# Optimization experiments

Hardware: AMD Instinct MI355X
Metric: run time of the kernel (lower is better)

## Reference

```python
import jax, jax.numpy as jnp
import numpy as np

STRIDES = (4, 8, 16, 32, 64)
RATIOS = (0.5, 1.0, 2.0)
SCALE = 8.0
A = 3
PRE_NMS = 2000
MAX_PER_IMG = 1000
NMS_THR = 0.7
MAX_RATIO = float(abs(np.log(16.0 / 1000.0)))  # wh_ratio_clip = 16/1000
LEVEL_OFFSET = 4096.0  # > max image coordinate, separates levels for batched NMS
FEAT_HW = ((208, 336), (104, 168), (52, 84), (26, 42), (13, 21))
N = 8


def grid_anchors(stride, H, W):
    # mmdet-style base anchors: scale 8, ratios (0.5,1,2), centered at 0
    r = jnp.asarray(RATIOS, jnp.float32)
    h_r = jnp.sqrt(r)
    w_r = 1.0 / h_r
    ws = stride * w_r * SCALE
    hs = stride * h_r * SCALE
    base = jnp.stack([-ws / 2, -hs / 2, ws / 2, hs / 2], axis=-1)  # [A,4]
    sx = jnp.arange(W, dtype=jnp.float32) * stride
    sy = jnp.arange(H, dtype=jnp.float32) * stride
    yy, xx = jnp.meshgrid(sy, sx, indexing='ij')
    shifts = jnp.stack([xx, yy, xx, yy], axis=-1).reshape(-1, 4)  # [H*W,4], row-major
    return (shifts[:, None, :] + base[None, :, :]).reshape(-1, 4)  # [H*W*A,4]


def decode(anchors, deltas, h, w):
    # DeltaXYWH decode with means 0, stds 1, clip to image
    px = (anchors[..., 0] + anchors[..., 2]) * 0.5
    py = (anchors[..., 1] + anchors[..., 3]) * 0.5
    pw = anchors[..., 2] - anchors[..., 0]
    ph = anchors[..., 3] - anchors[..., 1]
    dx, dy = deltas[..., 0], deltas[..., 1]
    dw = jnp.clip(deltas[..., 2], -MAX_RATIO, MAX_RATIO)
    dh = jnp.clip(deltas[..., 3], -MAX_RATIO, MAX_RATIO)
    gx = px + pw * dx
    gy = py + ph * dy
    gw = pw * jnp.exp(dw)
    gh = ph * jnp.exp(dh)
    x1 = jnp.clip(gx - gw * 0.5, 0.0, w)
    y1 = jnp.clip(gy - gh * 0.5, 0.0, h)
    x2 = jnp.clip(gx + gw * 0.5, 0.0, w)
    y2 = jnp.clip(gy + gh * 0.5, 0.0, h)
    return jnp.stack([x1, y1, x2, y2], axis=-1)


def iou_matrix(b):
    area = (b[:, 2] - b[:, 0]) * (b[:, 3] - b[:, 1])
    lt = jnp.maximum(b[:, None, :2], b[None, :, :2])
    rb = jnp.minimum(b[:, None, 2:], b[None, :, 2:])
    wh = jnp.clip(rb - lt, 0.0, None)
    inter = wh[..., 0] * wh[..., 1]
    union = area[:, None] + area[None, :] - inter
    return inter / jnp.maximum(union, 1e-6)


def _forward(cls_list, reg_list, image_h, image_w):
    scores_all, deltas_all, anchors_all, levels_all = [], [], [], []
    for lvl, (cls, reg) in enumerate(zip(cls_list, reg_list)):
        n, _, H, W = cls.shape
        anchors = grid_anchors(STRIDES[lvl], H, W)  # [H*W*A,4]
        s = jax.nn.sigmoid(jnp.transpose(cls, (0, 2, 3, 1)).reshape(n, -1))
        d = jnp.transpose(reg, (0, 2, 3, 1)).reshape(n, -1, 4)
        k = min(PRE_NMS, s.shape[1])  # topk pre-selection per level
        sv, si = jax.lax.top_k(s, k)
        dv = jnp.take_along_axis(d, si[..., None], axis=1)
        av = anchors[si]
        scores_all.append(sv)
        deltas_all.append(dv)
        anchors_all.append(av)
        levels_all.append(jnp.full((k,), lvl, jnp.int32))
    scores = jnp.concatenate(scores_all, axis=1)    # [N,M]
    deltas = jnp.concatenate(deltas_all, axis=1)    # [N,M,4]
    anchors = jnp.concatenate(anchors_all, axis=1)  # [N,M,4]
    levels = jnp.concatenate(levels_all)            # [M] (same per image)
    boxes = decode(anchors, deltas, float(image_h), float(image_w))
    # filter_boxes with min_area = prod((0,0)) = 0: keep boxes with area >= 0
    area = (boxes[..., 2] - boxes[..., 0]) * (boxes[..., 3] - boxes[..., 1])
    scores = jnp.where(area >= 0.0, scores, -1.0)
    M = boxes.shape[1]
    idxs = jnp.arange(M)

    def nms_one(bs):
        b_i, s_i = bs
        order = jnp.argsort(-s_i)
        b = b_i[order]
        s = s_i[order]
        lv = levels[order]
        # batched NMS: offset each level so cross-level boxes never overlap
        ob = jax.lax.stop_gradient(b + (lv.astype(b.dtype) * LEVEL_OFFSET)[:, None])
        iou = iou_matrix(ob)  # [M,M]

        def body(i, keep):
            sup = (iou[i] > NMS_THR) & (idxs > i) & keep[i]
            return keep & (~sup)

        keep = jax.lax.fori_loop(0, M, body, jnp.ones((M,), bool))
        rank = jnp.cumsum(keep.astype(jnp.int32)) - 1
        tgt = jnp.where(keep & (rank < MAX_PER_IMG), rank, MAX_PER_IMG)  # dump slot
        out_b = jnp.zeros((MAX_PER_IMG + 1, 4), b.dtype).at[tgt].set(b)[:MAX_PER_IMG]
        out_s = jnp.zeros((MAX_PER_IMG + 1,), s.dtype).at[tgt].set(s)[:MAX_PER_IMG]
        return out_b, out_s

    pb, ps = jax.lax.map(nms_one, (boxes, scores))  # sequential per image
    return pb, ps  # [N,1000,4], [N,1000] (zero-padded)


def setup_inputs() -> dict:
    key = jax.random.key(0)
    inp = {}
    for lvl, (H, W) in enumerate(FEAT_HW):
        k1 = jax.random.fold_in(key, 2 * lvl)
        k2 = jax.random.fold_in(key, 2 * lvl + 1)
        inp[f"class_out_{lvl}"] = jax.random.normal(k1, (N, A, H, W), jnp.float32)
        inp[f"reg_out_{lvl}"] = jax.random.normal(k2, (N, 4 * A, H, W), jnp.float32)
    inp["image_h"] = 832
    inp["image_w"] = 1344
    return inp


def reference(class_out_0, class_out_1, class_out_2, class_out_3, class_out_4,
              reg_out_0, reg_out_1, reg_out_2, reg_out_3, reg_out_4,
              image_h, image_w):
    cls_list = [class_out_0, class_out_1, class_out_2, class_out_3, class_out_4]
    reg_list = [reg_out_0, reg_out_1, reg_out_2, reg_out_3, reg_out_4]
    return _forward(cls_list, reg_list, image_h, image_w)
```

## Files before the change

kernel.cpp:

```cpp
#include <hip/hip_runtime.h>
#include <cmath>

#pragma clang fp contract(off)

namespace {
constexpr int NIMG = 8;
constexpr int NLVL = 5;
constexpr int LH[5]   = {208,104,52,26,13};
constexpr int LW[5]   = {336,168,84,42,21};
constexpr int LSTR[5] = {4,8,16,32,64};
constexpr int HWA[5]  = {209664,52416,13104,3276,819};
constexpr int KSEL[5] = {2000,2000,2000,2000,819};
constexpr int SOFF[5] = {0,2000,4000,6000,8000};
constexpr int MTOT    = 8819;
constexpr int CAP     = 6144;
constexpr int NPAIR   = NIMG*NLVL;
constexpr int CCUM[5] = {52,65,69,70,71};
constexpr int BLK_PER_IMG = 71;
constexpr int MASK_W  = 32;
constexpr int OUTK    = 1000;
constexpr int NT2[5]  = {272,272,272,272,55};

constexpr size_t OFF_HIST   = 0;
constexpr size_t OFF_PKC    = 0;
constexpr size_t OFF_CNT    = 655360;
constexpr size_t OFF_THR    = 655520;
constexpr size_t ZERO_BYTES = 655680;
constexpr size_t OFF_SELKEY = 1921120;
constexpr size_t OFF_SELBOX = 2767744;
constexpr size_t OFF_MASK   = 3896576;
constexpr size_t OFF_CKEY   = OFF_MASK;
constexpr size_t OFF_CBOX   = OFF_MASK + 2097152;
constexpr size_t OFF_KEEP   = 24376576;
}

struct Ins {
  const float* cls[5];
  const float* reg[5];
  const int* ih;
  const int* iw;
};

__device__ __forceinline__ void decode_block(int b, int& img, int& lvl, int& chunk) {
  img = b / BLK_PER_IMG;
  int rb = b - img*BLK_PER_IMG;
  if      (rb < CCUM[0]) { lvl=0; chunk=rb; }
  else if (rb < CCUM[1]) { lvl=1; chunk=rb-CCUM[0]; }
  else if (rb < CCUM[2]) { lvl=2; chunk=rb-CCUM[1]; }
  else if (rb < CCUM[3]) { lvl=3; chunk=rb-CCUM[2]; }
  else                   { lvl=4; chunk=0; }
}

__device__ __forceinline__ unsigned mapbits(float x) {
  unsigned u = __float_as_uint(x);
  return u ^ (unsigned)(((int)u >> 31) | (int)0x80000000);
}

__device__ __forceinline__ float sigmoid_ref(float x) {
  float e = (float)exp(-(double)x);
  return 1.0f / (1.0f + e);
}

__global__ void k_hist(Ins in, unsigned* __restrict__ hist) {
  int img, lvl, chunk; decode_block(blockIdx.x, img, lvl, chunk);
  __shared__ unsigned lh[4096];
  for (int i = threadIdx.x; i < 4096; i += 256) lh[i] = 0;
  __syncthreads();
  const float* src = in.cls[lvl] + (size_t)img * HWA[lvl];
  if (lvl != 4) {
    const float4* src4 = (const float4*)src;
    int nf4 = HWA[lvl] >> 2;
    int base4 = chunk * 1024;
    #pragma unroll
    for (int j = 0; j < 4; j++) {
      int f = base4 + j*256 + threadIdx.x;
      if (f < nf4) {
        float4 v = src4[f];
        atomicAdd(&lh[mapbits(v.x) >> 20], 1u);
        atomicAdd(&lh[mapbits(v.y) >> 20], 1u);
        atomicAdd(&lh[mapbits(v.z) >> 20], 1u);
        atomicAdd(&lh[mapbits(v.w) >> 20], 1u);
      }
    }
  } else {
    int base = chunk * 4096;
    #pragma unroll
    for (int j = 0; j < 16; j++) {
      int e = base + j*256 + threadIdx.x;
      if (e < HWA[4]) atomicAdd(&lh[mapbits(src[e]) >> 20], 1u);
    }
  }
  __syncthreads();
  unsigned* gh = hist + (img*NLVL + lvl) * 4096;
  for (int i = threadIdx.x; i < 4096; i += 256)
    if (lh[i]) atomicAdd(&gh[i], lh[i]);
}

__global__ void k_scan(const unsigned* __restrict__ hist, unsigned* __restrict__ thr) {
  int pair = blockIdx.x; int lvl = pair % NLVL;
  const unsigned* h = hist + (size_t)pair * 4096;
  __shared__ unsigned part[256];
  unsigned s = 0;
  #pragma unroll
  for (int i = 0; i < 16; i++) s += h[threadIdx.x*16 + i];
  part[threadIdx.x] = s;
  __syncthreads();
  if (threadIdx.x == 0) {
    unsigned k = (unsigned)KSEL[lvl];
    unsigned cum = 0;
    unsigned edge = 0;
    for (int t = 255; t >= 0; t--) {
      if (cum + part[t] >= k) {
        for (int b = t*16 + 15; b >= t*16; b--) {
          cum += h[b];
          if (cum >= k) { edge = (unsigned)b; break; }
        }
        thr[pair] = edge << 20;
        return;
      }
      cum += part[t];
    }
    thr[pair] = 0u;
  }
}

__global__ void __launch_bounds__(256) k_compact(Ins in, const unsigned* __restrict__ thr,
                          unsigned* __restrict__ cnt,
                          unsigned long long* __restrict__ ckey,
                          float4* __restrict__ cbox) {
  int img, lvl, chunk; decode_block(blockIdx.x, img, lvl, chunk);
  int pair = img*NLVL + lvl;
  unsigned T = thr[pair];
  const float* src = in.cls[lvl] + (size_t)img * HWA[lvl];
  int hw = LH[lvl] * LW[lvl];
  int lid = threadIdx.x & 63;
  __shared__ unsigned lbuf[4096];
  __shared__ unsigned long long lkey[4096];
  __shared__ unsigned lc, gbase;
  if (threadIdx.x == 0) lc = 0;
  __syncthreads();

  auto emit = [&](int e, float v, bool sel) {
    unsigned long long mask = __ballot(sel);
    if (mask != 0ull) {
      int leader = __ffsll((long long)mask) - 1;
      unsigned wb = 0;
      if (lid == leader) wb = atomicAdd(&lc, (unsigned)__popcll(mask));
      wb = (unsigned)__shfl((int)wb, leader, 64);
      if (sel) {
        unsigned p = wb + (unsigned)__popcll(mask & ((1ull << lid) - 1ull));
        int a = e / hw;
        int r = e - a*hw;
        unsigned idx = (unsigned)(r*3 + a);
        lbuf[p] = idx;
        float s = sigmoid_ref(v);
        unsigned pack = ((unsigned)lvl << 18) | idx;
        lkey[p] = ((unsigned long long)__float_as_uint(s) << 21)
                | (unsigned long long)(0x1FFFFFu - pack);
      }
    }
  };

  if (lvl != 4) {
    const float4* src4 = (const float4*)src;
    int nf4 = HWA[lvl] >> 2;
    int base4 = chunk * 1024;
    #pragma unroll
    for (int j = 0; j < 4; j++) {
      int f = base4 + j*256 + threadIdx.x;
      bool inb = f < nf4;
      float4 v4 = make_float4(0.f, 0.f, 0.f, 0.f);
      if (inb) v4 = src4[f];
      int e0 = f * 4;
      emit(e0+0, v4.x, inb && (mapbits(v4.x) >= T));
      emit(e0+1, v4.y, inb && (mapbits(v4.y) >= T));
      emit(e0+2, v4.z, inb && (mapbits(v4.z) >= T));
      emit(e0+3, v4.w, inb && (mapbits(v4.w) >= T));
    }
  } else {
    int base = chunk * 4096;
    #pragma unroll
    for (int j = 0; j < 16; j++) {
      int e = base + j*256 + threadIdx.x;
      float v = 0.0f;
      bool inb = (e < HWA[4]);
      if (inb) v = src[e];
      emit(e, v, inb && (mapbits(v) >= T));
    }
  }
  __syncthreads();
  if (threadIdx.x == 0) gbase = atomicAdd(&cnt[pair], lc);
  __syncthreads();
  unsigned nsel = lc, gb = gbase;
  float Wi = (float)(*in.iw), Hi = (float)(*in.ih);
  int Wl = LW[lvl];
  float st = (float)LSTR[lvl];
  const float* rg = in.reg[lvl] + (size_t)img * 4 * HWA[lvl];
  for (unsigned t = threadIdx.x; t < nsel; t += 256) {
    unsigned p = gb + t;
    if (p < CAP) {
      unsigned idx = lbuf[t];
      ckey[(size_t)pair*CAP + p] = lkey[t];
      int a = (int)(idx % 3u);
      int r = (int)(idx / 3u);
      int x = r % Wl, y = r / Wl;
      float dx = rg[(a*4+0)*hw + r];
      float dy = rg[(a*4+1)*hw + r];
      float dwv = rg[(a*4+2)*hw + r];
      float dhv = rg[(a*4+3)*hw + r];
      float ratio = (a==0) ? 0.5f : (a==1) ? 1.0f : 2.0f;
      float hr = sqrtf(ratio);
      float wr = 1.0f / hr;
      float wsz = st * wr * 8.0f;
      float hsz = st * hr * 8.0f;
      float xs = (float)x * st, ys = (float)y * st;
      float x1 = xs - wsz*0.5f, x2 = xs + wsz*0.5f;
      float y1 = ys - hsz*0.5f, y2 = ys + hsz*0.5f;
      float px = (x1 + x2) * 0.5f, py = (y1 + y2) * 0.5f;
      float pw = x2 - x1,          ph = y2 - y1;
      const float MR = 4.135166556742356f;
      dwv = fminf(fmaxf(dwv, -MR), MR);
      dhv = fminf(fmaxf(dhv, -MR), MR);
      float gx = px + pw*dx, gy = py + ph*dy;
      float gw = pw * (float)exp((double)dwv);
      float gh = ph * (float)exp((double)dhv);
      float4 bb;
      bb.x = fminf(fmaxf(gx - gw*0.5f, 0.0f), Wi);
      bb.y = fminf(fmaxf(gy - gh*0.5f, 0.0f), Hi);
      bb.z = fminf(fmaxf(gx + gw*0.5f, 0.0f), Wi);
      bb.w = fminf(fmaxf(gy + gh*0.5f, 0.0f), Hi);
      cbox[(size_t)pair*CAP + p] = bb;
    }
  }
}

__global__ void __launch_bounds__(256) k_rank(const unsigned* __restrict__ cntA,
                       const unsigned long long* __restrict__ ckey,
                       const float4* __restrict__ cbox,
                       unsigned long long* __restrict__ sel_key,
                       float* __restrict__ sel_box) {
  int pair = blockIdx.y; int tile = blockIdx.x;
  int img = pair / NLVL, lvl = pair % NLVL;
  int c = min((int)cntA[pair], CAP);
  if (tile*256 >= c) return;
  const unsigned long long* kp = ckey + (size_t)pair*CAP;
  int jj = tile*256 + threadIdx.x;
  bool act = jj < c;
  unsigned long long mykey = kp[min(jj, c-1)];
  int c_r = c & ~15;
  int r0 = 0, r1 = 0, r2 = 0, r3 = 0;
  for (int j0 = 0; j0 < c_r; j0 += 16) {
    #pragma unroll
    for (int u = 0; u < 16; u += 4) {
      r0 += (kp[j0+u  ] > mykey) ? 1 : 0;
      r1 += (kp[j0+u+1] > mykey) ? 1 : 0;
      r2 += (kp[j0+u+2] > mykey) ? 1 : 0;
      r3 += (kp[j0+u+3] > mykey) ? 1 : 0;
    }
  }
  int rk = r0 + r1 + r2 + r3;
  for (int j = c_r; j < c; j++) rk += (kp[j] > mykey) ? 1 : 0;
  if (act && rk < KSEL[lvl]) {
    int slot = img*MTOT + SOFF[lvl] + rk;
    sel_key[slot] = mykey;
    ((float4*)sel_box)[slot] = cbox[(size_t)pair*CAP + jj];
  }
}

__global__ void __launch_bounds__(256) k_masks(const float* __restrict__ sel_box,
                        unsigned long long* __restrict__ maskbuf) {
  int pair = blockIdx.y; int lvl = pair % NLVL; int img = pair / NLVL;
  int n = KSEL[lvl];
  int nw = (n + 63) >> 6;
  int nwc2 = (nw + 1) >> 1;
  int wv = threadIdx.x >> 6;
  int lane = threadIdx.x & 63;
  int t = blockIdx.x * 4 + wv;
  if (t >= NT2[lvl]) return;
  int rb = 0, cum = 0;
  while (cum + (nwc2 - (rb >> 1)) <= t) { cum += nwc2 - (rb >> 1); rb++; }
  int jw2 = (rb >> 1) + (t - cum);
  int jw0 = 2*jw2, jw1 = jw0 + 1;
  const float4* boxes = ((const float4*)sel_box) + img*MTOT + SOFF[lvl];
  float off = (float)lvl * 4096.0f;
  int c0 = jw0*64 + lane, c1 = c0 + 64;
  float b0x,b0y,b0z,b0w,a0, b1x,b1y,b1z,b1w,a1;
  if (c0 < n) {
    float4 b = boxes[c0];
    b0x = b.x + off; b0y = b.y + off; b0z = b.z + off; b0w = b.w + off;
    a0 = (b0z - b0x) * (b0w - b0y);
  } else { b0x=b0y=b0z=b0w=3.0e8f; a0=0.0f; }
  if (c1 < n) {
    float4 b = boxes[c1];
    b1x = b.x + off; b1y = b.y + off; b1z = b.z + off; b1w = b.w + off;
    a1 = (b1z - b1x) * (b1w - b1y);
  } else { b1x=b1y=b1z=b1w=3.0e8f; a1=0.0f; }
  __shared__ float4 sbox[4][64];
  __shared__ float  sarea[4][64];
  int row0 = rb*64;
  {
    float4 bi0 = boxes[min(row0 + lane, n-1)];
    bi0.x += off; bi0.y += off; bi0.z += off; bi0.w += off;
    sbox[wv][lane] = bi0;
    sarea[wv][lane] = (bi0.z - bi0.x) * (bi0.w - bi0.y);
  }
  bool z0 = (jw0 < rb);
  bool d0 = (jw0 == rb), d1 = (jw1 == rb);
  const float CHI = 0x1.66666ap-1f;
  const float CLO = 0x1.666664p-1f;
  unsigned long long acc0 = 0ull, acc1 = 0ull, unc = 0ull;
  #pragma unroll 16
  for (int r = 0; r < 64; r++) {
    float4 bi = sbox[wv][r];
    float ai = sarea[wv][r];
    float xx1 = fmaxf(bi.x, b0x), yy1 = fmaxf(bi.y, b0y);
    float xx2 = fminf(bi.z, b0z), yy2 = fminf(bi.w, b0w);
    float iw_ = fmaxf(xx2 - xx1, 0.0f), ih_ = fmaxf(yy2 - yy1, 0.0f);
    float in0 = iw_ * ih_;
    float u0 = fmaxf((ai + a0) - in0, 1e-6f);
    float xc1 = fmaxf(bi.x, b1x), yc1 = fmaxf(bi.y, b1y);
    float xc2 = fminf(bi.z, b1z), yc2 = fminf(bi.w, b1w);
    float jw_ = fmaxf(xc2 - xc1, 0.0f), jh_ = fmaxf(yc2 - yc1, 0.0f);
    float in1 = jw_ * jh_;
    float u1 = fmaxf((ai + a1) - in1, 1e-6f);
    unsigned long long h0 = __ballot(in0 >= CHI * u0);
    unsigned long long l0 = __ballot(in0 >= CLO * u0);
    unsigned long long h1 = __ballot(in1 >= CHI * u1);
    unsigned long long l1 = __ballot(in1 >= CLO * u1);
    unc |= (h0 ^ l0) | (h1 ^ l1);
    unsigned long long dm = ~((2ull << r) - 1ull);
    unsigned long long m0 = z0 ? 0ull : (d0 ? (h0 & dm) : h0);
    unsigned long long m1 = d1 ? (h1 & dm) : h1;
    if (lane == r) { acc0 = m0; acc1 = m1; }
  }
  if (unc) {
    const double Md = 0.70000001788139343261718750;
    acc0 = 0ull; acc1 = 0ull;
    #pragma unroll 1
    for (int r = 0; r < 64; r++) {
      float4 bi = sbox[wv][r];
      float ai = sarea[wv][r];
      float xx1 = fmaxf(bi.x, b0x), yy1 = fmaxf(bi.y, b0y);
      float xx2 = fminf(bi.z, b0z), yy2 = fminf(bi.w, b0w);
      float iw_ = fmaxf(xx2 - xx1, 0.0f), ih_ = fmaxf(yy2 - yy1, 0.0f);
      float in0 = iw_ * ih_;
      float u0 = fmaxf((ai + a0) - in0, 1e-6f);
      float xc1 = fmaxf(bi.x, b1x), yc1 = fmaxf(bi.y, b1y);
      float xc2 = fminf(bi.z, b1z), yc2 = fminf(bi.w, b1w);
      float jw_ = fmaxf(xc2 - xc1, 0.0f), jh_ = fmaxf(yc2 - yc1, 0.0f);
      float in1 = jw_ * jh_;
      float u1 = fmaxf((ai + a1) - in1, 1e-6f);
      unsigned long long w0 = __ballot((double)in0 >= Md * (double)u0);
      unsigned long long w1 = __ballot((double)in1 >= Md * (double)u1);
      unsigned long long dm = ~((2ull << r) - 1ull);
      unsigned long long m0 = z0 ? 0ull : (d0 ? (w0 & dm) : w0);
      unsigned long long m1 = d1 ? (w1 & dm) : w1;
      if (lane == r) { acc0 = m0; acc1 = m1; }
    }
  }
  int row = row0 + lane;
  if (row < n) {
    unsigned long long* dst = maskbuf + (size_t)pair*2000*MASK_W + (size_t)row*MASK_W + jw0;
    if (z0) {
      dst[1] = acc1;
    } else {
      ulonglong2 v; v.x = acc0; v.y = acc1;
      *((ulonglong2*)dst) = v;
    }
  }
}

__global__ void __launch_bounds__(1024) k_nms(const unsigned long long* __restrict__ maskbuf,
                      unsigned long long* __restrict__ keep, int* __restrict__ pkc) {
  int pair = blockIdx.x; int lvl = pair % NLVL;
  int n = KSEL[lvl];
  int nw = (n + 63) >> 6;
  const unsigned long long* mrow = maskbuf + (size_t)pair*2000*MASK_W;
  int tid = threadIdx.x;
  int w  = tid & 31;
  int rg = tid >> 5;
  __shared__ unsigned long long rem[32];
  __shared__ unsigned long long diag[64];
  __shared__ unsigned long long skw[32];
  __shared__ unsigned long long sSk;
  __shared__ int lcnt[64];
  if (tid < 32) { rem[tid] = 0ull; skw[tid] = 0ull; }
  __syncthreads();

  unsigned long long A0, A1, B0, B1;
  {
    int r0 = min(rg*2, n-1), r1 = min(rg*2+1, n-1);
    A0 = mrow[(size_t)r0*MASK_W + w];
    A1 = mrow[(size_t)r1*MASK_W + w];
  }
  for (int k = 0; k < nw; k++) {
    if (k + 1 < nw) {
      int r0 = min(64*(k+1) + rg*2, n-1), r1 = min(64*(k+1) + rg*2 + 1, n-1);
      B0 = mrow[(size_t)r0*MASK_W + w];
      B1 = mrow[(size_t)r1*MASK_W + w];
    }
    if (w == k) { diag[rg*2] = A0; diag[rg*2+1] = A1; }
    __syncthreads();
    if (tid < 64) {
      int row = 64*k + tid;
      bool valid = row < n;
      unsigned long long D = valid ? diag[tid] : 0ull;
      unsigned long long rk = rem[k];
      unsigned long long S = rk;
      for (int it = 0; it < 64; it++) {
        bool kept = valid && !((S >> tid) & 1ull);
        unsigned long long c = kept ? D : 0ull;
        #pragma unroll
        for (int m = 1; m < 64; m <<= 1) {
          unsigned lo = (unsigned)__shfl_xor((int)(unsigned)(c & 0xffffffffull), m, 64);
          unsigned hi = (unsigned)__shfl_xor((int)(unsigned)(c >> 32), m, 64);
          c |= ((unsigned long long)hi << 32) | (unsigned long long)lo;
        }
        unsigned long long Snew = rk | c;
        if (Snew == S) break;
        S = Snew;
      }
      if (tid == 0) {
        sSk = S;
        int nb = n - 64*k;
        unsigned long long vm = (nb >= 64) ? ~0ull : ((1ull << nb) - 1ull);
        unsigned long long kw = (~S) & vm;
        skw[k] = kw;
        keep[(size_t)pair*MASK_W + k] = kw;
      }
    }
    __syncthreads();
    if (w > k) {
      unsigned long long Sk = sSk;
      int r0 = 64*k + rg*2, r1 = r0 + 1;
      unsigned long long m = 0ull;
      if (r0 < n && !((Sk >> (rg*2)) & 1ull))     m |= A0;
      if (r1 < n && !((Sk >> (rg*2+1)) & 1ull))   m |= A1;
      if (m) atomicOr(&rem[w], m);
    }
    __syncthreads();
    A0 = B0; A1 = B1;
  }
  if (tid < 64) {
    int lane = tid;
    unsigned long long kw = (lane < nw) ? skw[lane] : 0ull;
    lcnt[lane] = __popcll(kw);
    int pre = 0;
    for (int t2 = 0; t2 < lane; t2++) pre += lcnt[t2];
    for (int b = 0; b < 64; b++) {
      int p = lane*64 + b;
      if (p < n) {
        pre += (int)((kw >> b) & 1ull);
        pkc[pair*2048 + p] = pre;
      }
    }
  }
}

__global__ void __launch_bounds__(256) k_out2(const unsigned long long* __restrict__ sel_key,
                      const float* __restrict__ sel_box,
                      const unsigned long long* __restrict__ keep,
                      const int* __restrict__ pkc,
                      float* __restrict__ out) {
  int img = blockIdx.y;
  int pos = blockIdx.x*256 + threadIdx.x;
  if (pos >= MTOT) return;
  int lvl = pos<2000?0 : pos<4000?1 : pos<6000?2 : pos<8000?3 : 4;
  int local = pos - SOFF[lvl];
  int pair = img*NLVL + lvl;
  unsigned long long kw = keep[(size_t)pair*MASK_W + (local >> 6)];
  if (!((kw >> (local & 63)) & 1ull)) return;
  unsigned long long mykey = sel_key[img*MTOT + pos];
  int rank = pkc[pair*2048 + local] - 1;
  #pragma unroll
  for (int l2 = 0; l2 < NLVL; l2++) {
    if (l2 == lvl) continue;
    const unsigned long long* A = sel_key + img*MTOT + SOFF[l2];
    int lo = 0, hi = KSEL[l2];
    while (lo < hi) {
      int mid = (lo + hi) >> 1;
      if (A[mid] > mykey) lo = mid + 1; else hi = mid;
    }
    if (lo > 0) rank += pkc[(img*NLVL + l2)*2048 + lo - 1];
  }
  if (rank < OUTK) {
    ((float4*)out)[img*OUTK + rank] = ((const float4*)sel_box)[img*MTOT + pos];
    out[NIMG*OUTK*4 + img*OUTK + rank] = __uint_as_float((unsigned)(mykey >> 21));
  }
}

extern "C" void kernel_launch(void* const* d_in, const int* in_sizes, int n_in,
                              void* d_out, int out_size, void* d_ws, size_t ws_size,
                              hipStream_t stream) {
  Ins in;
  for (int l = 0; l < 5; l++) {
    in.cls[l] = (const float*)d_in[2*l];
    in.reg[l] = (const float*)d_in[2*l + 1];
  }
  in.ih = (const int*)d_in[10];
  in.iw = (const int*)d_in[11];

  char* ws = (char*)d_ws;
  unsigned* hist              = (unsigned*)(ws + OFF_HIST);
  int* pkc                    = (int*)(ws + OFF_PKC);
  unsigned* cnt               = (unsigned*)(ws + OFF_CNT);
  unsigned* thr               = (unsigned*)(ws + OFF_THR);
  unsigned long long* sel_key = (unsigned long long*)(ws + OFF_SELKEY);
  float* sel_box              = (float*)(ws + OFF_SELBOX);
  unsigned long long* maskbuf = (unsigned long long*)(ws + OFF_MASK);
  unsigned long long* ckey    = (unsigned long long*)(ws + OFF_CKEY);
  float4* cbox                = (float4*)(ws + OFF_CBOX);
  unsigned long long* keep    = (unsigned long long*)(ws + OFF_KEEP);
  float* out                  = (float*)d_out;

  hipMemsetAsync(d_ws, 0, ZERO_BYTES, stream);
  hipMemsetAsync(d_out, 0, (size_t)NIMG*OUTK*5*sizeof(float), stream);

  k_hist   <<<NIMG*BLK_PER_IMG, 256, 0, stream>>>(in, hist);
  k_scan   <<<NPAIR, 256, 0, stream>>>(hist, thr);
  k_compact<<<NIMG*BLK_PER_IMG, 256, 0, stream>>>(in, thr, cnt, ckey, cbox);
  k_rank   <<<dim3(CAP/256, NPAIR), 256, 0, stream>>>(cnt, ckey, cbox, sel_key, sel_box);
  k_masks  <<<dim3(68, NPAIR), 256, 0, stream>>>(sel_box, maskbuf);
  k_nms    <<<NPAIR, 1024, 0, stream>>>(maskbuf, keep, pkc);
  k_out2   <<<dim3((MTOT + 255)/256, NIMG), 256, 0, stream>>>(sel_key, sel_box, keep, pkc, out);
}
```

Before: 286.8 us.

## Split rank computation into sliced shared-memory accumulation plus scatter kernel

```diff
diff --git a/kernel.cpp b/kernel.cpp
--- a/kernel.cpp
+++ b/kernel.cpp
@@ -25,7 +25,8 @@
 constexpr size_t OFF_PKC    = 0;
 constexpr size_t OFF_CNT    = 655360;
 constexpr size_t OFF_THR    = 655520;
-constexpr size_t ZERO_BYTES = 655680;
+constexpr size_t OFF_RNK    = 655872;
+constexpr size_t ZERO_BYTES = 1638912;
 constexpr size_t OFF_SELKEY = 1921120;
 constexpr size_t OFF_SELBOX = 2767744;
 constexpr size_t OFF_MASK   = 3896576;
@@ -234,35 +235,50 @@
   }
 }
 
-__global__ void __launch_bounds__(256) k_rank(const unsigned* __restrict__ cntA,
+__global__ void __launch_bounds__(256) k_racc(const unsigned* __restrict__ cntA,
+                       const unsigned long long* __restrict__ ckey,
+                       unsigned* __restrict__ rnk) {
+  int pair = blockIdx.z;
+  int c = min((int)cntA[pair], CAP);
+  int tile = blockIdx.x, slice = blockIdx.y;
+  if (tile*256 >= c || slice*256 >= c) return;
+  const unsigned long long* kp = ckey + (size_t)pair*CAP;
+  __shared__ unsigned long long sk[256];
+  int g = slice*256 + threadIdx.x;
+  sk[threadIdx.x] = (g < c) ? kp[g] : 0ull;
+  __syncthreads();
+  int jj = tile*256 + threadIdx.x;
+  unsigned long long mykey = kp[min(jj, c-1)];
+  const ulonglong2* sk2 = (const ulonglong2*)sk;
+  int r0 = 0, r1 = 0, r2 = 0, r3 = 0;
+  #pragma unroll 8
+  for (int j2 = 0; j2 < 128; j2 += 2) {
+    ulonglong2 a = sk2[j2];
+    ulonglong2 b = sk2[j2+1];
+    r0 += (a.x > mykey) ? 1 : 0;
+    r1 += (a.y > mykey) ? 1 : 0;
+    r2 += (b.x > mykey) ? 1 : 0;
+    r3 += (b.y > mykey) ? 1 : 0;
+  }
+  int rk = (r0 + r1) + (r2 + r3);
+  if (jj < c && rk) atomicAdd(&rnk[pair*CAP + jj], (unsigned)rk);
+}
+
+__global__ void __launch_bounds__(256) k_rsel(const unsigned* __restrict__ cntA,
                        const unsigned long long* __restrict__ ckey,
                        const float4* __restrict__ cbox,
+                       const unsigned* __restrict__ rnk,
                        unsigned long long* __restrict__ sel_key,
                        float* __restrict__ sel_box) {
   int pair = blockIdx.y; int tile = blockIdx.x;
   int img = pair / NLVL, lvl = pair % NLVL;
   int c = min((int)cntA[pair], CAP);
-  if (tile*256 >= c) return;
-  const unsigned long long* kp = ckey + (size_t)pair*CAP;
   int jj = tile*256 + threadIdx.x;
-  bool act = jj < c;
-  unsigned long long mykey = kp[min(jj, c-1)];
-  int c_r = c & ~15;
-  int r0 = 0, r1 = 0, r2 = 0, r3 = 0;
-  for (int j0 = 0; j0 < c_r; j0 += 16) {
-    #pragma unroll
-    for (int u = 0; u < 16; u += 4) {
-      r0 += (kp[j0+u  ] > mykey) ? 1 : 0;
-      r1 += (kp[j0+u+1] > mykey) ? 1 : 0;
-      r2 += (kp[j0+u+2] > mykey) ? 1 : 0;
-      r3 += (kp[j0+u+3] > mykey) ? 1 : 0;
-    }
-  }
-  int rk = r0 + r1 + r2 + r3;
-  for (int j = c_r; j < c; j++) rk += (kp[j] > mykey) ? 1 : 0;
-  if (act && rk < KSEL[lvl]) {
+  if (jj >= c) return;
+  int rk = (int)rnk[pair*CAP + jj];
+  if (rk < KSEL[lvl]) {
     int slot = img*MTOT + SOFF[lvl] + rk;
-    sel_key[slot] = mykey;
+    sel_key[slot] = ckey[(size_t)pair*CAP + jj];
     ((float4*)sel_box)[slot] = cbox[(size_t)pair*CAP + jj];
   }
 }
@@ -505,6 +521,7 @@
   int* pkc                    = (int*)(ws + OFF_PKC);
   unsigned* cnt               = (unsigned*)(ws + OFF_CNT);
   unsigned* thr               = (unsigned*)(ws + OFF_THR);
+  unsigned* rnk               = (unsigned*)(ws + OFF_RNK);
   unsigned long long* sel_key = (unsigned long long*)(ws + OFF_SELKEY);
   float* sel_box              = (float*)(ws + OFF_SELBOX);
   unsigned long long* maskbuf = (unsigned long long*)(ws + OFF_MASK);
@@ -519,7 +536,8 @@
   k_hist   <<<NIMG*BLK_PER_IMG, 256, 0, stream>>>(in, hist);
   k_scan   <<<NPAIR, 256, 0, stream>>>(hist, thr);
   k_compact<<<NIMG*BLK_PER_IMG, 256, 0, stream>>>(in, thr, cnt, ckey, cbox);
-  k_rank   <<<dim3(CAP/256, NPAIR), 256, 0, stream>>>(cnt, ckey, cbox, sel_key, sel_box);
+  k_racc   <<<dim3(CAP/256, CAP/256, NPAIR), 256, 0, stream>>>(cnt, ckey, rnk);
+  k_rsel   <<<dim3(CAP/256, NPAIR), 256, 0, stream>>>(cnt, ckey, cbox, rnk, sel_key, sel_box);
   k_masks  <<<dim3(68, NPAIR), 256, 0, stream>>>(sel_box, maskbuf);
   k_nms    <<<NPAIR, 1024, 0, stream>>>(maskbuf, keep, pkc);
   k_out2   <<<dim3((MTOT + 255)/256, NIMG), 256, 0, stream>>>(sel_key, sel_box, keep, pkc, out);
```

New measurement: 249.5 us. 1.15x faster.
